# Performance work log

Hardware: AMD Instinct MI355X
Metric: run time of the kernel (lower is better)

## Reference

```python
import jax, jax.numpy as jnp
import numpy as np

D_MODEL = 1024
N_HEADS = 16
DEPTH = D_MODEL // N_HEADS
P_FEAT = 64
NEG_BIG = -1.0e9


def setup_inputs() -> dict:
    key = jax.random.key(0)
    ks = jax.random.split(key, 12)
    B, S = 4, 2048
    s = 1.0 / np.sqrt(D_MODEL)
    return {
        "q": jax.random.normal(ks[0], (B, S, D_MODEL), jnp.float32),
        "k": jax.random.normal(ks[1], (B, S, D_MODEL), jnp.float32),
        "v": jax.random.normal(ks[2], (B, S, D_MODEL), jnp.float32),
        "protocol_features": jax.random.normal(ks[3], (B, P_FEAT), jnp.float32),
        "mask": jax.random.randint(ks[4], (B, 1, 1, S), 0, 2).astype(jnp.float32),
        "wq": jax.random.normal(ks[5], (D_MODEL, D_MODEL), jnp.float32) * s,
        "bq": jnp.zeros((D_MODEL,), jnp.float32),
        "wk": jax.random.normal(ks[6], (D_MODEL, D_MODEL), jnp.float32) * s,
        "bk": jnp.zeros((D_MODEL,), jnp.float32),
        "wv": jax.random.normal(ks[7], (D_MODEL, D_MODEL), jnp.float32) * s,
        "bv": jnp.zeros((D_MODEL,), jnp.float32),
        "wg": jax.random.normal(ks[8], (P_FEAT, N_HEADS), jnp.float32) * (1.0 / np.sqrt(P_FEAT)),
        "bg": jnp.zeros((N_HEADS,), jnp.float32),
    }


def _split_heads(x, B):
    # [B,S,d_model] -> [B,H,S,depth]
    return x.reshape(B, -1, N_HEADS, DEPTH).transpose(0, 2, 1, 3)


def reference(q, k, v, protocol_features, mask, wq, bq, wk, bk, wv, bv, wg, bg):
    B = q.shape[0]
    qh = _split_heads(q @ wq + bq, B)
    kh = _split_heads(k @ wk + bk, B)
    vh = _split_heads(v @ wv + bv, B)
    # scaled QK^T: [B,H,S,S]
    logits = jnp.einsum("bhqd,bhkd->bhqk", qh, kh) / jnp.sqrt(jnp.float32(DEPTH))
    # per-head protocol gate (sigmoid), broadcast over q/k positions
    validity = jax.nn.sigmoid(protocol_features @ wg + bg)  # [B,H]
    logits = logits * validity[:, :, None, None]
    logits = logits + mask * NEG_BIG
    attn = jax.nn.softmax(logits, axis=-1)
    out = jnp.einsum("bhqk,bhkd->bhqd", attn, vh)
    concat = out.transpose(0, 2, 1, 3).reshape(B, -1, D_MODEL)
    return concat, attn
```

## Files before the change

### kernel.cpp

```cpp
#include <hip/hip_runtime.h>

#define S_LEN 2048
#define NB 4
#define NH 16
#define BHN 64
#define DM 1024
#define DEP 64
#define MROWS 8192

typedef __attribute__((ext_vector_type(8))) short short8;
typedef __attribute__((ext_vector_type(4))) float f32x4;

#define MFMA_BF16(a, b, c) __builtin_amdgcn_mfma_f32_16x16x32_bf16((a), (b), (c), 0, 0, 0)

typedef __attribute__((address_space(1))) const void* as1cv;
typedef __attribute__((address_space(3))) void* as3v;

__device__ __forceinline__ void gld16(const void* g, void* l) {
  __builtin_amdgcn_global_load_lds((as1cv)g, (as3v)l, 16, 0, 0);
}

__device__ __forceinline__ unsigned short f2bf(float f) {
  unsigned u = __float_as_uint(f);
  u += 0x7fffu + ((u >> 16) & 1u);
  return (unsigned short)(u >> 16);
}

__device__ __forceinline__ unsigned cvtpk(float a, float b) {
  unsigned r;
  asm("v_cvt_pk_bf16_f32 %0, %1, %2" : "=v"(r) : "v"(a), "v"(b));
  return r;
}

__device__ __forceinline__ int SWZ(int row, int gran) {
  return row * 64 + ((gran ^ (row & 7)) << 3);
}

__global__ void gate_kernel(const float* __restrict__ pf, const float* __restrict__ wg,
                            const float* __restrict__ bg, float* __restrict__ validity) {
  int t = threadIdx.x;
  int b = t >> 4, h = t & 15;
  float s = bg[h];
  for (int i = 0; i < 64; i++) s += pf[b * 64 + i] * wg[i * NH + h];
  validity[t] = 1.0f / (1.0f + __expf(-s));
}

__global__ __launch_bounds__(256) void conv_bf16_kernel(const float* __restrict__ in,
                                                        unsigned short* __restrict__ out) {
  size_t i = ((size_t)blockIdx.x * 256 + threadIdx.x) * 8;
  float4 a = *(const float4*)(in + i);
  float4 b = *(const float4*)(in + i + 4);
  union { unsigned short us[8]; uint4 v; } o;
  o.us[0] = f2bf(a.x); o.us[1] = f2bf(a.y); o.us[2] = f2bf(a.z); o.us[3] = f2bf(a.w);
  o.us[4] = f2bf(b.x); o.us[5] = f2bf(b.y); o.us[6] = f2bf(b.z); o.us[7] = f2bf(b.w);
  *(uint4*)(out + i) = o.v;
}

__global__ __launch_bounds__(256) void wt_kernel(const float* __restrict__ W,
                                                 unsigned short* __restrict__ Wt) {
  __shared__ unsigned short T[64][72];
  int k0 = blockIdx.x * 64, n0 = blockIdx.y * 64;
  int t = threadIdx.x;
  int r = t >> 2, c4 = (t & 3) * 16;
  for (int j = 0; j < 16; j += 4) {
    float4 v = *(const float4*)&W[(size_t)(k0 + r) * DM + n0 + c4 + j];
    T[r][c4 + j + 0] = f2bf(v.x); T[r][c4 + j + 1] = f2bf(v.y);
    T[r][c4 + j + 2] = f2bf(v.z); T[r][c4 + j + 3] = f2bf(v.w);
  }
  __syncthreads();
  union { unsigned short us[16]; uint4 v[2]; } o;
  for (int j = 0; j < 16; j++) o.us[j] = T[c4 + j][r];
  *(uint4*)&Wt[(size_t)(n0 + r) * DM + k0 + c4] = o.v[0];
  *(uint4*)&Wt[(size_t)(n0 + r) * DM + k0 + c4 + 8] = o.v[1];
}

__global__ __launch_bounds__(256) void vt_kernel(const unsigned short* __restrict__ vh,
                                                 unsigned short* __restrict__ vhT) {
  __shared__ unsigned short T[64][72];
  int bh = blockIdx.y;
  int s0 = blockIdx.x * 64;
  int t = threadIdx.x;
  int r = t >> 2, c4 = (t & 3) * 16;
  const unsigned short* src = vh + ((size_t)bh * S_LEN + s0 + r) * DEP + c4;
  *(uint4*)&T[r][c4] = *(const uint4*)src;
  *(uint4*)&T[r][c4 + 8] = *(const uint4*)(src + 8);
  __syncthreads();
  union { unsigned short us[16]; uint4 v[2]; } o;
  for (int j = 0; j < 16; j++) o.us[j] = T[c4 + j][r];
  unsigned short* dst = vhT + ((size_t)bh * DEP + r) * S_LEN + s0 + c4;
  *(uint4*)dst = o.v[0];
  *(uint4*)(dst + 8) = o.v[1];
}

__global__ __launch_bounds__(256) void proj_gemm(const unsigned short* __restrict__ A,
                                                 const unsigned short* __restrict__ Bt,
                                                 const float* __restrict__ bias,
                                                 unsigned short* __restrict__ Y) {
  __shared__ unsigned short As[128 * 64], Bs[128 * 64];
  const int K = DM;
  int tid = threadIdx.x, w = tid >> 6, l = tid & 63, g = l >> 4, lc = l & 15;
  int r0 = blockIdx.x * 128, c0 = blockIdx.y * 128;
  int wr = w >> 1, wc = w & 1;
  int lrow = l >> 3, lcol = (l & 7) * 8;
  f32x4 acc[4][4] = {};
  for (int k0 = 0; k0 < K; k0 += 64) {
    __syncthreads();
    for (int i = 0; i < 4; i++) {
      int row = (w * 4 + i) * 8 + lrow;
      gld16(A + (size_t)(r0 + row) * K + k0 + lcol, &As[(w * 4 + i) * 512]);
      gld16(Bt + (size_t)(c0 + row) * K + k0 + lcol, &Bs[(w * 4 + i) * 512]);
    }
    __syncthreads();
    for (int kk = 0; kk < 2; kk++) {
      short8 a[4], b[4];
      for (int m = 0; m < 4; m++)
        a[m] = *(const short8*)&As[(wr * 64 + m * 16 + lc) * 64 + kk * 32 + g * 8];
      for (int n = 0; n < 4; n++)
        b[n] = *(const short8*)&Bs[(wc * 64 + n * 16 + lc) * 64 + kk * 32 + g * 8];
      for (int m = 0; m < 4; m++)
        for (int n = 0; n < 4; n++)
          acc[m][n] = MFMA_BF16(a[m], b[n], acc[m][n]);
    }
  }
  for (int n = 0; n < 4; n++) {
    int c = c0 + wc * 64 + n * 16 + lc;
    float bi = bias[c];
    int h = c >> 6, d = c & 63;
    for (int m = 0; m < 4; m++) {
      int rowbase = r0 + wr * 64 + m * 16 + g * 4;
      for (int r = 0; r < 4; r++) {
        int row = rowbase + r;
        int b_ = row >> 11, s = row & 2047;
        Y[(((size_t)b_ * NH + h) * S_LEN + s) * DEP + d] = f2bf(acc[m][n][r] + bi);
      }
    }
  }
}

__global__ __launch_bounds__(512) void attn_fused(const unsigned short* __restrict__ qh,
                                                  const unsigned short* __restrict__ kh,
                                                  const unsigned short* __restrict__ vhT,
                                                  const float* __restrict__ validity,
                                                  const float* __restrict__ mask,
                                                  float* __restrict__ concat,
                                                  float* __restrict__ attn) {
  __shared__ union {
    unsigned short Q[128 * 64];
    float PF[8][16 * 68];
  } QP;
  __shared__ unsigned short KV[4][64 * 64];
  __shared__ float Ms[S_LEN];

  int id = blockIdx.x;
  int cxcd = id & 7, j = id >> 3;
  int bh = cxcd * 8 + (j >> 4);
  int q0 = (j & 15) * 128;
  int b = bh >> 4, h = bh & 15;

  int tid = threadIdx.x, w = tid >> 6, l = tid & 63, g = l >> 4, lc = l & 15;
  int srow = l >> 3;
  int sgran = (l & 7) ^ srow;
  float scale = validity[bh] * 0.125f * 1.44269504f;
  for (int i = tid; i < S_LEN; i += 512)
    Ms[i] = mask[(size_t)b * S_LEN + i] * (-1.44269504e9f);

  const unsigned short* qb = qh + (size_t)bh * S_LEN * DEP;
  const unsigned short* kb = kh + (size_t)bh * S_LEN * DEP;
  const unsigned short* vb = vhT + (size_t)bh * DEP * S_LEN;
  int qrow = w * 16 + lc;

  unsigned short* B0 = &KV[0][0];
  unsigned short* B1 = &KV[2][0];
  for (int i = 0; i < 2; i++)
    gld16(qb + (size_t)(q0 + i * 64 + w * 8 + srow) * DEP + sgran * 8,
          &QP.Q[(i * 64 + w * 8) * 64]);
  for (int i = 0; i < 2; i++)
    gld16(kb + (size_t)(i * 64 + w * 8 + srow) * DEP + sgran * 8,
          B0 + (i * 64 + w * 8) * 64);
  __syncthreads();
  short8 aq0 = *(const short8*)&QP.Q[SWZ(qrow, g)];
  short8 aq1 = *(const short8*)&QP.Q[SWZ(qrow, 4 + g)];

  float ell[4] = {0.f, 0.f, 0.f, 0.f};
  for (int kt2 = 0; kt2 < 16; kt2++) {
    const int cb = kt2 & 1;
    unsigned short* cur = cb ? B1 : B0;
    if (kt2 < 15) {
      unsigned short* nxt = cb ? B0 : B1;
      for (int i = 0; i < 2; i++)
        gld16(kb + (size_t)((kt2 + 1) * 128 + i * 64 + w * 8 + srow) * DEP + sgran * 8,
              nxt + (i * 64 + w * 8) * 64);
    }
    __builtin_amdgcn_sched_barrier(0);
    if (kt2 < 15) { asm volatile("s_waitcnt vmcnt(2)" ::: "memory"); }
    else          { asm volatile("s_waitcnt vmcnt(0)" ::: "memory"); }
    __builtin_amdgcn_sched_barrier(0);
    for (int f = 0; f < 8; f++) {
      int krow = f * 16 + lc;
      short8 b0 = *(const short8*)&cur[SWZ(krow, g)];
      short8 b1 = *(const short8*)&cur[SWZ(krow, 4 + g)];
      f32x4 c = {};
      __builtin_amdgcn_s_setprio(1);
      c = MFMA_BF16(aq0, b0, c);
      c = MFMA_BF16(aq1, b1, c);
      __builtin_amdgcn_s_setprio(0);
      float mb = Ms[kt2 * 128 + f * 16 + lc];
      for (int r = 0; r < 4; r++) ell[r] += exp2f(fmaf(c[r], scale, mb));
    }
    __builtin_amdgcn_s_barrier();
  }
  for (int m = 8; m >= 1; m >>= 1)
    for (int r = 0; r < 4; r++) ell[r] += __shfl_xor(ell[r], m, 64);
  float rinv[4];
  for (int r = 0; r < 4; r++) rinv[r] = 1.0f / ell[r];

  gld16(kb + (size_t)(w * 8 + srow) * DEP + sgran * 8, &KV[0][w * 512]);
  gld16(vb + (size_t)(w * 8 + srow) * S_LEN + sgran * 8, &KV[2][w * 512]);
  __syncthreads();

  float* PFw = QP.PF[w];
  float* arow2 = attn + ((size_t)bh * S_LEN + q0 + w * 16 + lc) * S_LEN + g * 8;

  f32x4 O[4] = {};
#pragma unroll 2
  for (int kt = 0; kt < 32; kt++) {
    const int cb = kt & 1;
    if (kt < 31) {
      gld16(kb + (size_t)((kt + 1) * 64 + w * 8 + srow) * DEP + sgran * 8,
            &KV[cb ^ 1][w * 512]);
      gld16(vb + (size_t)(w * 8 + srow) * S_LEN + (kt + 1) * 64 + sgran * 8,
            &KV[2 + (cb ^ 1)][w * 512]);
    }
    __builtin_amdgcn_sched_barrier(0);
    if (kt < 31) { asm volatile("s_waitcnt vmcnt(6)" ::: "memory"); }
    else         { asm volatile("s_waitcnt vmcnt(4)" ::: "memory"); }
    __builtin_amdgcn_sched_barrier(0);
    for (int f = 0; f < 4; f++) {
      int krow = f * 16 + lc;
      short8 b0 = *(const short8*)&KV[cb][SWZ(krow, g)];
      short8 b1 = *(const short8*)&KV[cb][SWZ(krow, 4 + g)];
      f32x4 c = {};
      __builtin_amdgcn_s_setprio(1);
      c = MFMA_BF16(aq0, b0, c);
      c = MFMA_BF16(aq1, b1, c);
      __builtin_amdgcn_s_setprio(0);
      float mb = Ms[kt * 64 + f * 16 + lc];
      for (int r = 0; r < 4; r++) {
        float p = exp2f(fmaf(c[r], scale, mb)) * rinv[r];
        PFw[(g * 4 + r) * 68 + f * 16 + lc] = p;
      }
    }
    f32x4 t0 = *(const f32x4*)&PFw[lc * 68 + g * 8];
    f32x4 t1 = *(const f32x4*)&PFw[lc * 68 + g * 8 + 4];
    f32x4 t2 = *(const f32x4*)&PFw[lc * 68 + 32 + g * 8];
    f32x4 t3 = *(const f32x4*)&PFw[lc * 68 + 32 + g * 8 + 4];
    union { uint4 u; short8 s; } pk0, pk1;
    pk0.u = uint4{cvtpk(t0[0], t0[1]), cvtpk(t0[2], t0[3]),
                  cvtpk(t1[0], t1[1]), cvtpk(t1[2], t1[3])};
    pk1.u = uint4{cvtpk(t2[0], t2[1]), cvtpk(t2[2], t2[3]),
                  cvtpk(t3[0], t3[1]), cvtpk(t3[2], t3[3])};
    *(f32x4*)(arow2 + kt * 64) = t0;
    *(f32x4*)(arow2 + kt * 64 + 4) = t1;
    *(f32x4*)(arow2 + kt * 64 + 32) = t2;
    *(f32x4*)(arow2 + kt * 64 + 36) = t3;
    __builtin_amdgcn_s_setprio(1);
    for (int n = 0; n < 4; n++) {
      int vrow = n * 16 + lc;
      short8 v0 = *(const short8*)&KV[2 + cb][SWZ(vrow, g)];
      short8 v1 = *(const short8*)&KV[2 + cb][SWZ(vrow, 4 + g)];
      O[n] = MFMA_BF16(pk0.s, v0, O[n]);
      O[n] = MFMA_BF16(pk1.s, v1, O[n]);
    }
    __builtin_amdgcn_s_setprio(0);
    __builtin_amdgcn_s_barrier();
  }
  for (int n = 0; n < 4; n++)
    for (int r = 0; r < 4; r++)
      concat[((size_t)b * S_LEN + q0 + w * 16 + g * 4 + r) * DM + h * DEP + n * 16 + lc] =
          O[n][r];
}

extern "C" void kernel_launch(void* const* d_in, const int* in_sizes, int n_in,
                              void* d_out, int out_size, void* d_ws, size_t ws_size,
                              hipStream_t stream) {
  const float* q    = (const float*)d_in[0];
  const float* k    = (const float*)d_in[1];
  const float* v    = (const float*)d_in[2];
  const float* pf   = (const float*)d_in[3];
  const float* mask = (const float*)d_in[4];
  const float* wq   = (const float*)d_in[5];
  const float* bq   = (const float*)d_in[6];
  const float* wk   = (const float*)d_in[7];
  const float* bk   = (const float*)d_in[8];
  const float* wv   = (const float*)d_in[9];
  const float* bv   = (const float*)d_in[10];
  const float* wg   = (const float*)d_in[11];
  const float* bg   = (const float*)d_in[12];

  float* concat = (float*)d_out;
  float* attn   = concat + (size_t)NB * S_LEN * DM;

  unsigned short* qbf = (unsigned short*)attn;
  unsigned short* kbf = qbf + (size_t)MROWS * DM;
  unsigned short* vbf = kbf + (size_t)MROWS * DM;
  unsigned short* wqT = vbf + (size_t)MROWS * DM;
  unsigned short* wkT = wqT + (size_t)DM * DM;
  unsigned short* wvT = wkT + (size_t)DM * DM;

  float* validity = (float*)d_ws;
  unsigned short* qhp = (unsigned short*)((char*)d_ws + 4096);
  unsigned short* khp = qhp + (size_t)MROWS * DM;
  unsigned short* vhp = khp + (size_t)MROWS * DM;
  unsigned short* vhT = vhp + (size_t)MROWS * DM;

  gate_kernel<<<1, 64, 0, stream>>>(pf, wg, bg, validity);

  conv_bf16_kernel<<<4096, 256, 0, stream>>>(q, qbf);
  conv_bf16_kernel<<<4096, 256, 0, stream>>>(k, kbf);
  conv_bf16_kernel<<<4096, 256, 0, stream>>>(v, vbf);

  wt_kernel<<<dim3(16, 16), 256, 0, stream>>>(wq, wqT);
  wt_kernel<<<dim3(16, 16), 256, 0, stream>>>(wk, wkT);
  wt_kernel<<<dim3(16, 16), 256, 0, stream>>>(wv, wvT);

  proj_gemm<<<dim3(64, 8), 256, 0, stream>>>(qbf, wqT, bq, qhp);
  proj_gemm<<<dim3(64, 8), 256, 0, stream>>>(kbf, wkT, bk, khp);
  proj_gemm<<<dim3(64, 8), 256, 0, stream>>>(vbf, wvT, bv, vhp);

  vt_kernel<<<dim3(32, 64), 256, 0, stream>>>(vhp, vhT);

  attn_fused<<<1024, 512, 0, stream>>>(qhp, khp, vhT, validity, mask, concat, attn);
}
```

Baseline: 504.8 us.

## Fuse fp32-to-bf16 input conversion into a batched QKV projection GEMM

Removes the three standalone conversion kernels and has the projection GEMM read fp32 activations directly, converting to bf16 while staging tiles into shared memory. The three Q/K/V projections are merged into a single launch using blockIdx.z. This avoids writing and re-reading the bf16 activation copies and cuts launches. In exchange, the A-tile load becomes a synchronous register path instead of the async global-to-LDS load, and each GEMM block reads twice as many bytes for A, so the GEMM may see more load latency.

```diff
diff --git a/kernel.cpp b/kernel.cpp
--- a/kernel.cpp
+++ b/kernel.cpp
@@ -43,17 +43,6 @@
   float s = bg[h];
   for (int i = 0; i < 64; i++) s += pf[b * 64 + i] * wg[i * NH + h];
   validity[t] = 1.0f / (1.0f + __expf(-s));
-}
-
-__global__ __launch_bounds__(256) void conv_bf16_kernel(const float* __restrict__ in,
-                                                        unsigned short* __restrict__ out) {
-  size_t i = ((size_t)blockIdx.x * 256 + threadIdx.x) * 8;
-  float4 a = *(const float4*)(in + i);
-  float4 b = *(const float4*)(in + i + 4);
-  union { unsigned short us[8]; uint4 v; } o;
-  o.us[0] = f2bf(a.x); o.us[1] = f2bf(a.y); o.us[2] = f2bf(a.z); o.us[3] = f2bf(a.w);
-  o.us[4] = f2bf(b.x); o.us[5] = f2bf(b.y); o.us[6] = f2bf(b.z); o.us[7] = f2bf(b.w);
-  *(uint4*)(out + i) = o.v;
 }
 
 __global__ __launch_bounds__(256) void wt_kernel(const float* __restrict__ W,
@@ -92,23 +81,42 @@
   *(uint4*)(dst + 8) = o.v[1];
 }
 
-__global__ __launch_bounds__(256) void proj_gemm(const unsigned short* __restrict__ A,
-                                                 const unsigned short* __restrict__ Bt,
-                                                 const float* __restrict__ bias,
-                                                 unsigned short* __restrict__ Y) {
+__global__ __launch_bounds__(256) void proj3_gemm(const float* __restrict__ Xq,
+                                                  const float* __restrict__ Xk,
+                                                  const float* __restrict__ Xv,
+                                                  const unsigned short* __restrict__ BtBase,
+                                                  const float* __restrict__ bq,
+                                                  const float* __restrict__ bk,
+                                                  const float* __restrict__ bv,
+                                                  unsigned short* __restrict__ Ybase) {
   __shared__ unsigned short As[128 * 64], Bs[128 * 64];
   const int K = DM;
+  int z = blockIdx.z;
+  const float* X = (z == 0) ? Xq : (z == 1) ? Xk : Xv;
+  const float* bias = (z == 0) ? bq : (z == 1) ? bk : bv;
+  const unsigned short* Bt = BtBase + (size_t)z * DM * DM;
+  unsigned short* Y = Ybase + (size_t)z * MROWS * DM;
+
   int tid = threadIdx.x, w = tid >> 6, l = tid & 63, g = l >> 4, lc = l & 15;
   int r0 = blockIdx.x * 128, c0 = blockIdx.y * 128;
   int wr = w >> 1, wc = w & 1;
   int lrow = l >> 3, lcol = (l & 7) * 8;
+  int sr = tid >> 3, sc = (tid & 7) * 8;
   f32x4 acc[4][4] = {};
   for (int k0 = 0; k0 < K; k0 += 64) {
     __syncthreads();
     for (int i = 0; i < 4; i++) {
       int row = (w * 4 + i) * 8 + lrow;
-      gld16(A + (size_t)(r0 + row) * K + k0 + lcol, &As[(w * 4 + i) * 512]);
       gld16(Bt + (size_t)(c0 + row) * K + k0 + lcol, &Bs[(w * 4 + i) * 512]);
+    }
+    for (int i = 0; i < 4; i++) {
+      int row = i * 32 + sr;
+      const float* src = X + (size_t)(r0 + row) * K + k0 + sc;
+      float4 a0 = *(const float4*)src;
+      float4 a1 = *(const float4*)(src + 4);
+      uint4 o = {cvtpk(a0.x, a0.y), cvtpk(a0.z, a0.w),
+                 cvtpk(a1.x, a1.y), cvtpk(a1.z, a1.w)};
+      *(uint4*)&As[row * 64 + sc] = o;
     }
     __syncthreads();
     for (int kk = 0; kk < 2; kk++) {
@@ -300,10 +308,7 @@
   float* concat = (float*)d_out;
   float* attn   = concat + (size_t)NB * S_LEN * DM;
 
-  unsigned short* qbf = (unsigned short*)attn;
-  unsigned short* kbf = qbf + (size_t)MROWS * DM;
-  unsigned short* vbf = kbf + (size_t)MROWS * DM;
-  unsigned short* wqT = vbf + (size_t)MROWS * DM;
+  unsigned short* wqT = (unsigned short*)attn;
   unsigned short* wkT = wqT + (size_t)DM * DM;
   unsigned short* wvT = wkT + (size_t)DM * DM;
 
@@ -315,17 +320,11 @@
 
   gate_kernel<<<1, 64, 0, stream>>>(pf, wg, bg, validity);
 
-  conv_bf16_kernel<<<4096, 256, 0, stream>>>(q, qbf);
-  conv_bf16_kernel<<<4096, 256, 0, stream>>>(k, kbf);
-  conv_bf16_kernel<<<4096, 256, 0, stream>>>(v, vbf);
-
   wt_kernel<<<dim3(16, 16), 256, 0, stream>>>(wq, wqT);
   wt_kernel<<<dim3(16, 16), 256, 0, stream>>>(wk, wkT);
   wt_kernel<<<dim3(16, 16), 256, 0, stream>>>(wv, wvT);
 
-  proj_gemm<<<dim3(64, 8), 256, 0, stream>>>(qbf, wqT, bq, qhp);
-  proj_gemm<<<dim3(64, 8), 256, 0, stream>>>(kbf, wkT, bk, khp);
-  proj_gemm<<<dim3(64, 8), 256, 0, stream>>>(vbf, wvT, bv, vhp);
+  proj3_gemm<<<dim3(64, 8, 3), 256, 0, stream>>>(q, k, v, wqT, bq, bk, bv, qhp);
 
   vt_kernel<<<dim3(32, 64), 256, 0, stream>>>(vhp, vhT);
 
```

Result: faster. 480.0 us (-4.9%).
